# Performance work log

Hardware: AMD Instinct MI355X
Metric: run time of the kernel (lower is better)

Reference implementation:

```python
import jax, jax.numpy as jnp
import numpy as np

NEG_SLOPE = 0.2
K_L = 0.5
K_G = 0.5
TEMP_G = 1e-3


def _leaky(v):
    return jnp.where(v >= 0, v, NEG_SLOPE * v)


def _topk_row_mask(scores, keep):
    # scores: [n, n, h]; torch.topk(dim=0) -> indices [keep, n] per head,
    # then head_mask[indices, :] = 1 selects whole ROWS (any column hit).
    n = scores.shape[0]
    s = jnp.transpose(scores, (1, 2, 0))        # [n_cols, h, n_rows]
    _, idx = jax.lax.top_k(s, keep)             # [n_cols, h, keep]

    def per_head(idx_h):                        # idx_h: [n_cols, keep]
        return jnp.zeros((n,), scores.dtype).at[idx_h.reshape(-1)].set(1.0)

    rows = jax.vmap(per_head, in_axes=1, out_axes=0)(idx)  # [h, n_rows]
    return jnp.transpose(rows)[:, None, :]      # [n_rows, 1, h] broadcast over cols


def setup_inputs() -> dict:
    key = jax.random.key(0)
    ks = jax.random.split(key, 8)
    n, in_f, feat_dim = 1024, 256, 128
    H, F = 4, 64                                # n_heads, n_hidden (out_features=256)
    feats = jax.random.normal(ks[0], (n, feat_dim), dtype=jnp.float32)
    x = jax.random.normal(ks[1], (n, in_f), dtype=jnp.float32)
    adj = jax.random.randint(ks[2], (n, n, 1), 0, 2).astype(jnp.int32)
    sc = 0.05
    W_l = jax.random.normal(ks[3], (in_f, H * F), dtype=jnp.float32) * sc
    W_r = jax.random.normal(ks[4], (in_f, H * F), dtype=jnp.float32) * sc
    attn_w = jax.random.normal(ks[5], (F,), dtype=jnp.float32) * sc
    W_delta = jax.random.normal(ks[6], (2 * F, F), dtype=jnp.float32) * sc
    b_delta = jnp.zeros((F,), dtype=jnp.float32)
    return {"feats": feats, "x": x, "adj": adj, "W_l": W_l, "W_r": W_r,
            "attn_w": attn_w, "W_delta": W_delta, "b_delta": b_delta}


def reference(feats, x, adj, W_l, W_r, attn_w, W_delta, b_delta):
    n = x.shape[0]
    F = attn_w.shape[0]
    H = W_l.shape[1] // F
    g_l = (x @ W_l).reshape(n, H, F)
    g_r = (x @ W_r).reshape(n, H, F)
    # g_sum[i, j] = g_l[j] + g_r[i]  (repeat vs repeat_interleave ordering)
    g_sum = g_r[:, None, :, :] + g_l[None, :, :, :]          # [n, n, H, F]
    e = jnp.einsum('ijhf,f->ijh', _leaky(g_sum), attn_w)     # [n, n, H]

    mask_adj = adj > 0                                        # [n, n, 1]
    a_l = jax.nn.softmax(jnp.where(mask_adj, e, -jnp.inf), axis=1)
    a_1nd = a_l * mask_adj.astype(e.dtype)

    keep_l = int(n * (1.0 - K_L))
    a_filt = a_1nd * _topk_row_mask(a_1nd, keep_l)
    attn_local = jnp.einsum('ijh,jhf->ihf', a_filt, g_r)     # [n, H, F]

    omega = jax.nn.softmax(e, axis=1)
    fn = (feats - feats.min(axis=0)) / (feats.max(axis=0) - feats.min(axis=0))
    fn = jnp.where(jnp.isnan(fn), 0.0, fn)
    g_rn = (g_r - g_r.min(axis=0)) / (g_r.max(axis=0) - g_r.min(axis=0))
    nf = jnp.linalg.norm(fn, axis=1)                          # [n] (index j)
    ng = jnp.linalg.norm(g_rn, axis=2)                        # [n, H] (index i)
    alpha = jax.nn.softmax(jnp.abs(nf[None, :, None] - ng[:, None, :]), axis=1)
    gamma = 0.5 * (omega + (1.0 - alpha))

    keep_g = int(n * (1.0 - K_G))
    gf = gamma * _topk_row_mask(gamma, keep_g)
    gf = jax.nn.softmax(jnp.where(gf == 0, 1e-10, gf) / TEMP_G, axis=1)
    attn_global = jnp.einsum('ijh,jhf->ihf', gf, g_r)         # [n, H, F]

    inter = _leaky(jnp.concatenate([attn_local, attn_global], axis=2) @ W_delta + b_delta)
    delta = jax.nn.softmax(inter, axis=1)                     # softmax over heads (torch dim=1)
    attn_res = delta * attn_local + (1.0 - delta) * attn_global
    return attn_res.reshape(n, H * F)
```

## Files before the change

### kernel.cpp

```cpp
#include <hip/hip_runtime.h>
#include <cstdint>
#include <cstddef>

#define N 1024
#define HN 4
#define FDIM 64
#define KSEL 512
#define FLT_MAX_ 3.402823466e+38f

__device__ __forceinline__ float wred_sum(float v){
#pragma unroll
  for(int o=32;o>0;o>>=1) v += __shfl_down(v,o,64);
  return v;
}
__device__ __forceinline__ float bfly_sum(float v){
#pragma unroll
  for(int o=1;o<64;o<<=1) v += __shfl_xor(v,o,64);
  return v;
}
__device__ __forceinline__ float bfly_max(float v){
#pragma unroll
  for(int o=1;o<64;o<<=1) v = fmaxf(v,__shfl_xor(v,o,64));
  return v;
}
__device__ __forceinline__ float bred_sum(float v, float* scr){
  int t=threadIdx.x;
  v = wred_sum(v);
  __syncthreads();
  if((t&63)==0) scr[t>>6]=v;
  __syncthreads();
  return (scr[0]+scr[1])+(scr[2]+scr[3]);
}

__global__ __launch_bounds__(256) void stage1(const float* __restrict__ x,
                                              const float* __restrict__ W_l,
                                              const float* __restrict__ W_r,
                                              const int* __restrict__ adj,
                                              const float* __restrict__ feats,
                                              float* __restrict__ g_l,
                                              float* __restrict__ g_r,
                                              unsigned* __restrict__ adjbit,
                                              int* __restrict__ masks,
                                              float* __restrict__ pmin_f,
                                              float* __restrict__ pmax_f){
  int bx = blockIdx.x, t = threadIdx.x;
  if(bx < 512){
    const float* __restrict__ W = (bx >= 256) ? W_r : W_l;
    float* __restrict__ g = (bx >= 256) ? g_r : g_l;
    int i0 = (bx & 255)*4;
    float acc[4] = {0.f,0.f,0.f,0.f};
#pragma unroll 8
    for(int k=0;k<256;k++){
      float w = W[(size_t)k*256 + t];
#pragma unroll
      for(int r=0;r<4;r++) acc[r] = fmaf(x[(size_t)(i0+r)*256 + k], w, acc[r]);
    }
#pragma unroll
    for(int r=0;r<4;r++) g[(size_t)(i0+r)*256 + t] = acc[r];
  } else if(bx < 1536){
    int i = bx - 512, w = t>>6, lane = t&63;
    if(i < 32) masks[i*256 + t] = 0;
#pragma unroll
    for(int it=0; it<4; it++){
      int j = w*256 + it*64 + lane;
      int v = adj[(size_t)i*N + j];
      unsigned long long mb = __ballot(v > 0);
      if(lane == 0){
        adjbit[i*32 + w*8 + it*2]     = (unsigned)mb;
        adjbit[i*32 + w*8 + it*2 + 1] = (unsigned)(mb >> 32);
      }
    }
  } else {
    int chunk = bx - 1536;
    if(t < 128){
      float lo = FLT_MAX_, hi = -FLT_MAX_;
      int r0 = chunk*64;
      for(int r=0;r<64;r++){
        float v = feats[(size_t)(r0+r)*128 + t];
        lo = fminf(lo,v); hi = fmaxf(hi,v);
      }
      pmin_f[chunk*128+t]=lo; pmax_f[chunk*128+t]=hi;
    }
  }
}

__global__ __launch_bounds__(256) void stage2(const float* __restrict__ g_l,
                                              const float* __restrict__ g_r,
                                              const float* __restrict__ attn_w,
                                              const float* __restrict__ feats,
                                              const float* __restrict__ pmin_f, const float* __restrict__ pmax_f,
                                              float* __restrict__ pmin_g, float* __restrict__ pmax_g,
                                              float* __restrict__ psum_g,
                                              float* __restrict__ nf,
                                              float* __restrict__ e,
                                              float* __restrict__ eT){
  __shared__ __align__(16) float smem[2*64*68 + 128];
  int bx = blockIdx.x, t = threadIdx.x;
  if(bx < 1024){
    float* grs = smem;
    float* gls = smem + 64*68;
    float* aw  = smem + 2*64*68;
    float* aw2 = aw + 64;
    int h = bx >> 8, i0 = ((bx>>4)&15)*64, j0 = (bx&15)*64;
    if(t < 64){ float w = attn_w[t]; aw[t]=w; aw2[t]=0.2f*w; }
#pragma unroll
    for(int k=0;k<4;k++){
      int v = t + k*256;
      int r = v >> 4, f4 = (v & 15)*4;
      *(float4*)&grs[r*68 + f4] = *(const float4*)&g_r[(size_t)(i0+r)*256 + h*64 + f4];
      *(float4*)&gls[r*68 + f4] = *(const float4*)&g_l[(size_t)(j0+r)*256 + h*64 + f4];
    }
    __syncthreads();
    int tj = t&15, ti = t>>4;
    float acc[4][4];
#pragma unroll
    for(int a=0;a<4;a++)
#pragma unroll
      for(int b=0;b<4;b++) acc[a][b]=0.f;
    for(int fc=0; fc<64; fc+=4){
      float4 wv  = *(float4*)&aw[fc];
      float4 wv2 = *(float4*)&aw2[fc];
      float4 ga4[4], gb4[4];
#pragma unroll
      for(int a=0;a<4;a++) ga4[a] = *(float4*)&grs[(ti*4+a)*68+fc];
#pragma unroll
      for(int b=0;b<4;b++) gb4[b] = *(float4*)&gls[(tj+16*b)*68+fc];
#pragma unroll
      for(int a=0;a<4;a++)
#pragma unroll
        for(int b=0;b<4;b++){
          float s0 = ga4[a].x + gb4[b].x;
          float s1 = ga4[a].y + gb4[b].y;
          float s2 = ga4[a].z + gb4[b].z;
          float s3 = ga4[a].w + gb4[b].w;
          acc[a][b] = fmaf(s0, (s0>=0.f)?wv.x:wv2.x, acc[a][b]);
          acc[a][b] = fmaf(s1, (s1>=0.f)?wv.y:wv2.y, acc[a][b]);
          acc[a][b] = fmaf(s2, (s2>=0.f)?wv.z:wv2.z, acc[a][b]);
          acc[a][b] = fmaf(s3, (s3>=0.f)?wv.w:wv2.w, acc[a][b]);
        }
    }
#pragma unroll
    for(int a=0;a<4;a++)
#pragma unroll
      for(int b=0;b<4;b++){
        int i = i0 + ti*4 + a, j = j0 + tj + 16*b;
        e[((size_t)h*N + i)*N + j] = acc[a][b];
      }
    __syncthreads();
    float* esT = smem;
#pragma unroll
    for(int a=0;a<4;a++)
#pragma unroll
      for(int b=0;b<4;b++)
        esT[(tj + 16*b)*68 + ti*4 + a] = acc[a][b];
    __syncthreads();
#pragma unroll
    for(int k=0;k<4;k++){
      int jl = (t>>4) + 16*k, ilx = (t&15)*4;
      *(float4*)(eT + ((size_t)h*N + j0 + jl)*N + i0 + ilx) = *(float4*)&esT[jl*68 + ilx];
    }
  } else if(bx < 1040){
    int chunk = bx - 1024;
    float lo = FLT_MAX_, hi = -FLT_MAX_, sm = 0.f;
    int r0 = chunk*64;
    for(int r=0;r<64;r++){
      float v = g_r[(size_t)(r0+r)*256 + t];
      lo = fminf(lo,v); hi = fmaxf(hi,v); sm += v;
    }
    pmin_g[chunk*256+t]=lo; pmax_g[chunk*256+t]=hi; psum_g[chunk*256+t]=sm;
  } else {
    int i = bx - 1040;
    float* scr = smem;
    float u = 0.f;
    if(t < 128){
      float lo = FLT_MAX_, hi = -FLT_MAX_;
#pragma unroll
      for(int k=0;k<16;k++){
        lo = fminf(lo, pmin_f[k*128+t]);
        hi = fmaxf(hi, pmax_f[k*128+t]);
      }
      float d = hi - lo;
      float v = feats[(size_t)i*128 + t];
      u = (d==0.f) ? 0.f : (v - lo)/d;
    }
    float tot = bred_sum(u*u, scr);
    if(t==0) nf[i] = sqrtf(tot);
  }
}

__global__ __launch_bounds__(256) void row_stats(const float* __restrict__ e,
                                                 const unsigned* __restrict__ adjbit,
                                                 const float* __restrict__ nf,
                                                 const float* __restrict__ g_r,
                                                 const float* __restrict__ pmin_g, const float* __restrict__ pmax_g,
                                                 float* __restrict__ ng,
                                                 float* __restrict__ mlA, float* __restrict__ islA,
                                                 float* __restrict__ moA, float* __restrict__ isoA,
                                                 float* __restrict__ maA, float* __restrict__ isaA,
                                                 float* __restrict__ mgA, float* __restrict__ sgA){
  int i = blockIdx.x, t = threadIdx.x, h = t>>6, lane = t&63;
  float glo = FLT_MAX_, ghi = -FLT_MAX_;
#pragma unroll
  for(int k=0;k<16;k++){
    glo = fminf(glo, pmin_g[k*256 + h*64 + lane]);
    ghi = fmaxf(ghi, pmax_g[k*256 + h*64 + lane]);
  }
  float dg = ghi - glo;
  float ug = (g_r[(size_t)i*256 + h*64 + lane] - glo)/dg;
  float ngv = sqrtf(bfly_sum(ug*ug));
  if(lane==0) ng[h*N + i] = ngv;

  size_t base = ((size_t)h*N + i)*N;
  float er[16], nfr[16];
  unsigned nib[4];
#pragma unroll
  for(int c=0;c<4;c++){
    float4 e4 = *(const float4*)(e  + base + c*256 + lane*4);
    float4 n4 = *(const float4*)(nf + c*256 + lane*4);
    er[c*4+0]=e4.x; er[c*4+1]=e4.y; er[c*4+2]=e4.z; er[c*4+3]=e4.w;
    nfr[c*4+0]=n4.x; nfr[c*4+1]=n4.y; nfr[c*4+2]=n4.z; nfr[c*4+3]=n4.w;
    nib[c] = (adjbit[i*32 + c*8 + (lane>>3)] >> ((lane&7)*4)) & 0xFu;
  }
  float ml=-FLT_MAX_, mo=-FLT_MAX_, ma=-FLT_MAX_;
#pragma unroll
  for(int c=0;c<4;c++)
#pragma unroll
    for(int k=0;k<4;k++){
      int q = c*4+k;
      float ev = er[q];
      mo = fmaxf(mo, ev);
      if((nib[c]>>k)&1) ml = fmaxf(ml, ev);
      ma = fmaxf(ma, fabsf(nfr[q]-ngv));
    }
#pragma unroll
  for(int o=1;o<64;o<<=1){
    ml = fmaxf(ml, __shfl_xor(ml,o,64));
    mo = fmaxf(mo, __shfl_xor(mo,o,64));
    ma = fmaxf(ma, __shfl_xor(ma,o,64));
  }
  float sl=0.f, so=0.f, sa=0.f;
#pragma unroll
  for(int c=0;c<4;c++)
#pragma unroll
    for(int k=0;k<4;k++){
      int q = c*4+k;
      float ev = er[q];
      so += __expf(ev-mo);
      if((nib[c]>>k)&1) sl += __expf(ev-ml);
      sa += __expf(fabsf(nfr[q]-ngv)-ma);
    }
#pragma unroll
  for(int o=1;o<64;o<<=1){
    sl += __shfl_xor(sl,o,64);
    so += __shfl_xor(so,o,64);
    sa += __shfl_xor(sa,o,64);
  }
  float isl = 1.f/sl, iso = 1.f/so, isa = 1.f/sa;
  float gg[16];
  float mg = -FLT_MAX_;
#pragma unroll
  for(int q=0;q<16;q++){
    float ev = er[q];
    float omega = __expf(ev-mo)*iso;
    float alpha = __expf(fabsf(nfr[q]-ngv)-ma)*isa;
    float g = 0.5f*(omega + 1.f - alpha);
    gg[q] = g;
    mg = fmaxf(mg, g);
  }
  mg = bfly_max(mg);
  float sg = 0.f;
#pragma unroll
  for(int q=0;q<16;q++) sg += __expf((gg[q]-mg)/1e-3f);
  sg = bfly_sum(sg);
  if(lane==0){
    mlA[h*N+i]=ml; islA[h*N+i]=isl;
    moA[h*N+i]=mo; isoA[h*N+i]=iso;
    maA[h*N+i]=ma; isaA[h*N+i]=isa;
    mgA[h*N+i]=mg; sgA[h*N+i]=sg;
  }
}

__device__ __forceinline__ void apply_mask(const unsigned* ur, unsigned T, int tneed, int EQ,
                                           int* __restrict__ mask, int base, int lane){
  if(EQ == tneed){
#pragma unroll
    for(int c=0;c<4;c++)
#pragma unroll
      for(int k2=0;k2<4;k2++){
        int i = c*256 + lane*4 + k2;
        if(ur[c*4+k2] >= T) mask[base + i] = 1;
      }
  } else {
    int run_base = 0;
#pragma unroll
    for(int c=0;c<4;c++){
      unsigned long long bm[4];
#pragma unroll
      for(int k2=0;k2<4;k2++) bm[k2] = __ballot(ur[c*4+k2]==T);
      unsigned long long lower = (lane==0) ? 0ull : (~0ull >> (64-lane));
      int run = run_base;
#pragma unroll
      for(int k2=0;k2<4;k2++) run += (int)__popcll(bm[k2] & lower);
#pragma unroll
      for(int k2=0;k2<4;k2++){
        int i = c*256 + lane*4 + k2;
        unsigned u = ur[c*4+k2];
        bool sel = (u > T) || (u == T && run < tneed);
        run += (u==T)?1:0;
        if(sel) mask[base + i] = 1;
      }
      int ctot = 0;
#pragma unroll
      for(int k2=0;k2<4;k2++) ctot += (int)__popcll(bm[k2]);
      run_base += ctot;
    }
  }
}

__device__ __forceinline__ void run_select(const unsigned* ur, int* __restrict__ mask,
                                           int base, int lane){
  unsigned prefix = 0u;
  for(int b=30; b>=0; b--){
    unsigned cand = prefix | (1u<<b);
    int c = 0;
#pragma unroll
    for(int q=0;q<16;q++) c += (int)__popcll(__ballot(ur[q] >= cand));
    prefix = (c >= KSEL) ? cand : prefix;
  }
  unsigned T = prefix;
  int GT = 0, EQ = 0;
#pragma unroll
  for(int q=0;q<16;q++){
    GT += (int)__popcll(__ballot(ur[q] > T));
    EQ += (int)__popcll(__ballot(ur[q] == T));
  }
  int tneed = KSEL - GT;
  apply_mask(ur, T, tneed, EQ, mask, base, lane);
}

__global__ __launch_bounds__(256) void mm_sel(const float* __restrict__ eT,
                                              const float* __restrict__ g_r,
                                              const unsigned* __restrict__ adjbit,
                                              const float* __restrict__ nf,
                                              const float* __restrict__ mlA, const float* __restrict__ islA,
                                              const float* __restrict__ moA, const float* __restrict__ isoA,
                                              const float* __restrict__ maA, const float* __restrict__ isaA,
                                              const float* __restrict__ ngA,
                                              const float* __restrict__ mgA, const float* __restrict__ sgA,
                                              float* __restrict__ partL,
                                              float* __restrict__ partG,
                                              int* __restrict__ mask_l,
                                              int* __restrict__ mask_g){
  __shared__ __align__(16) float a_t[32][36];
  __shared__ __align__(16) float p_t[32][36];
  __shared__ __align__(16) float b_s[32][68];
  int bx = blockIdx.x, h = blockIdx.y, s = blockIdx.z;
  int t = threadIdx.x;

  if(bx < 64){
    int w = t>>6, lane = t&63;
    int sid = bx + 64*(h + 4*s);
    int gcol = sid*4 + w;
    int z  = gcol >> 12;
    int hj = gcol & 4095;
    int hh = hj >> 10, jc = hj & 1023;
    const float* __restrict__ src = eT + (size_t)hj * (size_t)N;

    float ev[16];
#pragma unroll
    for(int c=0;c<4;c++){
      float4 e4 = ((const float4*)src)[c*64 + lane];
      ev[c*4+0]=e4.x; ev[c*4+1]=e4.y; ev[c*4+2]=e4.z; ev[c*4+3]=e4.w;
    }
    unsigned ur[16];
    if(z == 0){
      int wo = jc >> 5; unsigned bm = 1u << (jc & 31);
#pragma unroll
      for(int c=0;c<4;c++){
        int ib = (hh<<10) + c*256 + lane*4;
        float4 ml4 = *(const float4*)(mlA+ib);
        float4 il4 = *(const float4*)(islA+ib);
        float mlv[4] = {ml4.x,ml4.y,ml4.z,ml4.w};
        float ilv[4] = {il4.x,il4.y,il4.z,il4.w};
#pragma unroll
        for(int k=0;k<4;k++){
          int i = c*256 + lane*4 + k;
          float a = (adjbit[i*32 + wo] & bm) ? __expf(ev[c*4+k]-mlv[k])*ilv[k] : 0.f;
          ur[c*4+k] = __float_as_uint(a);
        }
      }
      run_select(ur, mask_l, hh<<10, lane);
    } else {
      float nfv = nf[jc];
#pragma unroll
      for(int c=0;c<4;c++){
        int ib = (hh<<10) + c*256 + lane*4;
        float4 mo4 = *(const float4*)(moA+ib);
        float4 io4 = *(const float4*)(isoA+ib);
        float4 ma4 = *(const float4*)(maA+ib);
        float4 ia4 = *(const float4*)(isaA+ib);
        float4 ng4 = *(const float4*)(ngA+ib);
        float mov[4]={mo4.x,mo4.y,mo4.z,mo4.w}, iov[4]={io4.x,io4.y,io4.z,io4.w};
        float mav[4]={ma4.x,ma4.y,ma4.z,ma4.w}, iav[4]={ia4.x,ia4.y,ia4.z,ia4.w};
        float ngv[4]={ng4.x,ng4.y,ng4.z,ng4.w};
#pragma unroll
        for(int k=0;k<4;k++){
          float omega = __expf(ev[c*4+k]-mov[k])*iov[k];
          float alpha = __expf(fabsf(nfv-ngv[k])-mav[k])*iav[k];
          float g = 0.5f*(omega + 1.f - alpha);
          ur[c*4+k] = __float_as_uint(g);
        }
      }
      run_select(ur, mask_g, hh<<10, lane);
    }
    return;
  }

  int i0 = (bx-64)*32, j0 = s*128;
  int il = t & 31, jq = t >> 5;
  int gi = h*N + i0 + il;
  float ml_r = mlA[gi], il_r = islA[gi];
  float mo_r = moA[gi], io_r = isoA[gi];
  float ma_r = maA[gi], ia_r = isaA[gi];
  float ng_r = ngA[gi];
  float mg_r = mgA[gi], isg_r = 1.f/sgA[gi];
  int fq = t & 15, iq = t >> 4;
  int jb2a = t>>4, d4a = t&15;
  int idxb = t + 256, jb2b = idxb>>4, d4b = idxb&15;

  float e0,e1,e2,e3; unsigned aw; float4 nf4, vb0, vb1;
  {
    int jb = j0;
    size_t ebase = ((size_t)h*N + jb + jq*4)*(size_t)N + i0 + il;
    e0 = eT[ebase]; e1 = eT[ebase+N]; e2 = eT[ebase+2*N]; e3 = eT[ebase+3*N];
    aw = adjbit[(size_t)(i0+il)*32 + s*4 + 0];
    nf4 = *(const float4*)(nf + jb + jq*4);
    vb0 = *(const float4*)(g_r + (size_t)(jb+jb2a)*256 + h*64 + d4a*4);
    vb1 = *(const float4*)(g_r + (size_t)(jb+jb2b)*256 + h*64 + d4b*4);
  }
  float4 accL[2], accG[2];
#pragma unroll
  for(int r=0;r<2;r++){ accL[r]=make_float4(0,0,0,0); accG[r]=make_float4(0,0,0,0); }

  for(int sub=0; sub<4; sub++){
    __syncthreads();
    {
      float evs[4] = {e0,e1,e2,e3};
      float nfsv[4] = {nf4.x,nf4.y,nf4.z,nf4.w};
#pragma unroll
      for(int c=0;c<4;c++){
        int jl = jq*4 + c;
        float a = ((aw >> jl) & 1u) ? __expf(evs[c]-ml_r)*il_r : 0.f;
        float omega = __expf(evs[c]-mo_r)*io_r;
        float alpha = __expf(fabsf(nfsv[c]-ng_r)-ma_r)*ia_r;
        float g = 0.5f*(omega + 1.f - alpha);
        float p = __expf((g-mg_r)/1e-3f)*isg_r;
        a_t[jl][il] = a;
        p_t[jl][il] = p;
      }
      *(float4*)&b_s[jb2a][d4a*4] = vb0;
      *(float4*)&b_s[jb2b][d4b*4] = vb1;
    }
    if(sub < 3){
      int jb = j0 + (sub+1)*32;
      size_t ebase = ((size_t)h*N + jb + jq*4)*(size_t)N + i0 + il;
      e0 = eT[ebase]; e1 = eT[ebase+N]; e2 = eT[ebase+2*N]; e3 = eT[ebase+3*N];
      aw = adjbit[(size_t)(i0+il)*32 + s*4 + sub + 1];
      nf4 = *(const float4*)(nf + jb + jq*4);
      vb0 = *(const float4*)(g_r + (size_t)(jb+jb2a)*256 + h*64 + d4a*4);
      vb1 = *(const float4*)(g_r + (size_t)(jb+jb2b)*256 + h*64 + d4b*4);
    }
    __syncthreads();
#pragma unroll 8
    for(int j=0;j<32;j++){
      float4 bv = *(float4*)&b_s[j][fq*4];
      float2 av = *(float2*)&a_t[j][iq*2];
      float2 pv = *(float2*)&p_t[j][iq*2];
      accL[0].x = fmaf(av.x, bv.x, accL[0].x); accL[0].y = fmaf(av.x, bv.y, accL[0].y);
      accL[0].z = fmaf(av.x, bv.z, accL[0].z); accL[0].w = fmaf(av.x, bv.w, accL[0].w);
      accL[1].x = fmaf(av.y, bv.x, accL[1].x); accL[1].y = fmaf(av.y, bv.y, accL[1].y);
      accL[1].z = fmaf(av.y, bv.z, accL[1].z); accL[1].w = fmaf(av.y, bv.w, accL[1].w);
      accG[0].x = fmaf(pv.x, bv.x, accG[0].x); accG[0].y = fmaf(pv.x, bv.y, accG[0].y);
      accG[0].z = fmaf(pv.x, bv.z, accG[0].z); accG[0].w = fmaf(pv.x, bv.w, accG[0].w);
      accG[1].x = fmaf(pv.y, bv.x, accG[1].x); accG[1].y = fmaf(pv.y, bv.y, accG[1].y);
      accG[1].z = fmaf(pv.y, bv.z, accG[1].z); accG[1].w = fmaf(pv.y, bv.w, accG[1].w);
    }
  }
#pragma unroll
  for(int r=0;r<2;r++){
    int i = i0 + iq*2 + r;
    size_t o = ((size_t)s*N + i)*256 + h*64 + fq*4;
    *(float4*)&partL[o] = accL[r];
    *(float4*)&partG[o] = accG[r];
  }
}

__global__ __launch_bounds__(256) void epilogue(const float* __restrict__ partL,
                                                const float* __restrict__ partG,
                                                const int* __restrict__ mask_l,
                                                const int* __restrict__ mask_g,
                                                const float* __restrict__ psum_g,
                                                const float* __restrict__ W_delta,
                                                const float* __restrict__ b_delta,
                                                float* __restrict__ out){
  __shared__ float cat[4][128];
  __shared__ float inter_s[4][64];
  int i = blockIdx.x, t = threadIdx.x;
  int h = t>>6, f = t&63;
  float sl = 0.f, sg = 0.f;
#pragma unroll
  for(int s2=0;s2<8;s2++){
    size_t o = ((size_t)s2*N + i)*256 + h*64 + f;
    sl += partL[o];
    sg += partG[o];
  }
  if(!mask_l[h*N + i]) sl = 0.f;
  if(!mask_g[h*N + i]){
    float gs = 0.f;
#pragma unroll
    for(int k=0;k<16;k++) gs += psum_g[k*256 + t];
    sg = gs * (1.f/1024.f);
  }
  cat[h][f]      = sl;
  cat[h][64 + f] = sg;
  __syncthreads();
  float d = b_delta[f];
#pragma unroll 8
  for(int c=0;c<128;c++) d = fmaf(cat[h][c], W_delta[(size_t)c*64 + f], d);
  d = (d >= 0.f) ? d : 0.2f*d;
  inter_s[h][f] = d;
  __syncthreads();
  float m = inter_s[0][f];
#pragma unroll
  for(int hh=1;hh<4;hh++) m = fmaxf(m, inter_s[hh][f]);
  float ssum = 0.f;
#pragma unroll
  for(int hh=0;hh<4;hh++) ssum += __expf(inter_s[hh][f]-m);
  float delta = __expf(d - m)/ssum;
  out[(size_t)i*256 + h*64 + f] = delta*sl + (1.f - delta)*sg;
}

extern "C" void kernel_launch(void* const* d_in, const int* in_sizes, int n_in,
                              void* d_out, int out_size, void* d_ws, size_t ws_size,
                              hipStream_t stream) {
  const float* feats  = (const float*)d_in[0];
  const float* x      = (const float*)d_in[1];
  const int*   adj    = (const int*)  d_in[2];
  const float* W_l    = (const float*)d_in[3];
  const float* W_r    = (const float*)d_in[4];
  const float* attn_w = (const float*)d_in[5];
  const float* W_delta= (const float*)d_in[6];
  const float* b_delta= (const float*)d_in[7];
  float* out = (float*)d_out;

  float* ws = (float*)d_ws;
  size_t off = 0;
  float* g_l   = ws+off; off += (size_t)N*256;
  float* g_r   = ws+off; off += (size_t)N*256;
  float* e     = ws+off; off += (size_t)HN*N*N;
  float* eT    = ws+off; off += (size_t)HN*N*N;
  float* partL = ws+off; off += (size_t)8*N*256;
  float* partG = ws+off; off += (size_t)8*N*256;
  float* pmin_f= ws+off; off += 16*128;
  float* pmax_f= ws+off; off += 16*128;
  float* pmin_g= ws+off; off += 16*256;
  float* pmax_g= ws+off; off += 16*256;
  float* psum_g= ws+off; off += 16*256;
  float* nf    = ws+off; off += N;
  float* ng    = ws+off; off += (size_t)HN*N;
  float* mlA   = ws+off; off += (size_t)HN*N;
  float* islA  = ws+off; off += (size_t)HN*N;
  float* moA   = ws+off; off += (size_t)HN*N;
  float* isoA  = ws+off; off += (size_t)HN*N;
  float* maA   = ws+off; off += (size_t)HN*N;
  float* isaA  = ws+off; off += (size_t)HN*N;
  float* mgA   = ws+off; off += (size_t)HN*N;
  float* sgA   = ws+off; off += (size_t)HN*N;
  int* mask_l  = (int*)(ws+off); off += (size_t)HN*N;
  int* mask_g  = (int*)(ws+off); off += (size_t)HN*N;
  unsigned* adjbit = (unsigned*)(ws+off); off += (size_t)N*32;

  stage1<<<1552, 256, 0, stream>>>(x, W_l, W_r, adj, feats, g_l, g_r, adjbit, mask_l, pmin_f, pmax_f);

  stage2<<<2064, 256, 0, stream>>>(g_l, g_r, attn_w, feats, pmin_f, pmax_f,
                                   pmin_g, pmax_g, psum_g, nf, e, eT);

  row_stats<<<N, 256, 0, stream>>>(e, adjbit, nf, g_r, pmin_g, pmax_g, ng,
                                   mlA, islA, moA, isoA, maA, isaA, mgA, sgA);

  mm_sel<<<dim3(96,HN,8), 256, 0, stream>>>(eT, g_r, adjbit, nf,
                                            mlA, islA, moA, isoA, maA, isaA, ng,
                                            mgA, sgA, partL, partG, mask_l, mask_g);

  epilogue<<<N, 256, 0, stream>>>(partL, partG, mask_l, mask_g, psum_g, W_delta, b_delta, out);
}
```

Before: 184.6 us.

## Add transposed adjacency bitmask, stage e stores through LDS, reorder mm_sel blocks

Builds a column-major adjacency bitmask in extra stage2 blocks so the selection path in mm_sel reads one coalesced word per 32 rows instead of a strided bit per row. The row-major e tile is now staged in shared memory and written as float4 alongside eT, replacing scattered scalar stores. mm_sel's block ordering is flipped so matmul blocks get the low indices and selection blocks the high ones. This adds 16 blocks that reread the full int adjacency matrix and a second bitmask buffer.

```diff
diff --git a/kernel.cpp b/kernel.cpp
--- a/kernel.cpp
+++ b/kernel.cpp
@@ -88,10 +88,12 @@
                                               const float* __restrict__ g_r,
                                               const float* __restrict__ attn_w,
                                               const float* __restrict__ feats,
+                                              const int* __restrict__ adj,
                                               const float* __restrict__ pmin_f, const float* __restrict__ pmax_f,
                                               float* __restrict__ pmin_g, float* __restrict__ pmax_g,
                                               float* __restrict__ psum_g,
                                               float* __restrict__ nf,
+                                              unsigned* __restrict__ adjbitT,
                                               float* __restrict__ e,
                                               float* __restrict__ eT){
   __shared__ __align__(16) float smem[2*64*68 + 128];
@@ -139,25 +141,22 @@
           acc[a][b] = fmaf(s3, (s3>=0.f)?wv.w:wv2.w, acc[a][b]);
         }
     }
+    __syncthreads();
+    float* es  = smem;
+    float* esT = smem + 64*68;
 #pragma unroll
     for(int a=0;a<4;a++)
 #pragma unroll
       for(int b=0;b<4;b++){
-        int i = i0 + ti*4 + a, j = j0 + tj + 16*b;
-        e[((size_t)h*N + i)*N + j] = acc[a][b];
+        es [(ti*4+a)*68 + (tj+16*b)] = acc[a][b];
+        esT[(tj+16*b)*68 + (ti*4+a)] = acc[a][b];
       }
     __syncthreads();
-    float* esT = smem;
-#pragma unroll
-    for(int a=0;a<4;a++)
-#pragma unroll
-      for(int b=0;b<4;b++)
-        esT[(tj + 16*b)*68 + ti*4 + a] = acc[a][b];
-    __syncthreads();
 #pragma unroll
     for(int k=0;k<4;k++){
-      int jl = (t>>4) + 16*k, ilx = (t&15)*4;
-      *(float4*)(eT + ((size_t)h*N + j0 + jl)*N + i0 + ilx) = *(float4*)&esT[jl*68 + ilx];
+      int rl = (t>>4) + 16*k, cl4 = (t&15)*4;
+      *(float4*)(e  + ((size_t)h*N + i0 + rl)*N + j0 + cl4) = *(float4*)&es [rl*68 + cl4];
+      *(float4*)(eT + ((size_t)h*N + j0 + rl)*N + i0 + cl4) = *(float4*)&esT[rl*68 + cl4];
     }
   } else if(bx < 1040){
     int chunk = bx - 1024;
@@ -168,7 +167,7 @@
       lo = fminf(lo,v); hi = fmaxf(hi,v); sm += v;
     }
     pmin_g[chunk*256+t]=lo; pmax_g[chunk*256+t]=hi; psum_g[chunk*256+t]=sm;
-  } else {
+  } else if(bx < 2064){
     int i = bx - 1040;
     float* scr = smem;
     float u = 0.f;
@@ -185,6 +184,19 @@
     }
     float tot = bred_sum(u*u, scr);
     if(t==0) nf[i] = sqrtf(tot);
+  } else {
+    int B = bx - 2064, j0 = B*64;
+    int w = t>>6, lane = t&63;
+    unsigned word = 0u;
+    for(int ii=0; ii<256; ii++){
+      int i = w*256 + ii;
+      int v = adj[(size_t)i*N + j0 + lane];
+      word |= (v > 0 ? 1u : 0u) << (ii & 31);
+      if((ii & 31) == 31){
+        adjbitT[(size_t)(j0+lane)*32 + (i>>5)] = word;
+        word = 0u;
+      }
+    }
   }
 }
 
@@ -341,6 +353,7 @@
 __global__ __launch_bounds__(256) void mm_sel(const float* __restrict__ eT,
                                               const float* __restrict__ g_r,
                                               const unsigned* __restrict__ adjbit,
+                                              const unsigned* __restrict__ adjbitT,
                                               const float* __restrict__ nf,
                                               const float* __restrict__ mlA, const float* __restrict__ islA,
                                               const float* __restrict__ moA, const float* __restrict__ isoA,
@@ -357,9 +370,9 @@
   int bx = blockIdx.x, h = blockIdx.y, s = blockIdx.z;
   int t = threadIdx.x;
 
-  if(bx < 64){
+  if(bx >= 32){
     int w = t>>6, lane = t&63;
-    int sid = bx + 64*(h + 4*s);
+    int sid = (bx - 32) + 64*(h + 4*s);
     int gcol = sid*4 + w;
     int z  = gcol >> 12;
     int hj = gcol & 4095;
@@ -374,9 +387,10 @@
     }
     unsigned ur[16];
     if(z == 0){
-      int wo = jc >> 5; unsigned bm = 1u << (jc & 31);
+      size_t tbase = (size_t)jc*32;
 #pragma unroll
       for(int c=0;c<4;c++){
+        unsigned awT = adjbitT[tbase + c*8 + (lane>>3)];
         int ib = (hh<<10) + c*256 + lane*4;
         float4 ml4 = *(const float4*)(mlA+ib);
         float4 il4 = *(const float4*)(islA+ib);
@@ -384,8 +398,7 @@
         float ilv[4] = {il4.x,il4.y,il4.z,il4.w};
 #pragma unroll
         for(int k=0;k<4;k++){
-          int i = c*256 + lane*4 + k;
-          float a = (adjbit[i*32 + wo] & bm) ? __expf(ev[c*4+k]-mlv[k])*ilv[k] : 0.f;
+          float a = ((awT >> ((lane&7)*4 + k)) & 1u) ? __expf(ev[c*4+k]-mlv[k])*ilv[k] : 0.f;
           ur[c*4+k] = __float_as_uint(a);
         }
       }
@@ -416,7 +429,7 @@
     return;
   }
 
-  int i0 = (bx-64)*32, j0 = s*128;
+  int i0 = bx*32, j0 = s*128;
   int il = t & 31, jq = t >> 5;
   int gi = h*N + i0 + il;
   float ml_r = mlA[gi], il_r = islA[gi];
@@ -578,17 +591,18 @@
   float* sgA   = ws+off; off += (size_t)HN*N;
   int* mask_l  = (int*)(ws+off); off += (size_t)HN*N;
   int* mask_g  = (int*)(ws+off); off += (size_t)HN*N;
-  unsigned* adjbit = (unsigned*)(ws+off); off += (size_t)N*32;
+  unsigned* adjbit  = (unsigned*)(ws+off); off += (size_t)N*32;
+  unsigned* adjbitT = (unsigned*)(ws+off); off += (size_t)N*32;
 
   stage1<<<1552, 256, 0, stream>>>(x, W_l, W_r, adj, feats, g_l, g_r, adjbit, mask_l, pmin_f, pmax_f);
 
-  stage2<<<2064, 256, 0, stream>>>(g_l, g_r, attn_w, feats, pmin_f, pmax_f,
-                                   pmin_g, pmax_g, psum_g, nf, e, eT);
+  stage2<<<2080, 256, 0, stream>>>(g_l, g_r, attn_w, feats, adj, pmin_f, pmax_f,
+                                   pmin_g, pmax_g, psum_g, nf, adjbitT, e, eT);
 
   row_stats<<<N, 256, 0, stream>>>(e, adjbit, nf, g_r, pmin_g, pmax_g, ng,
                                    mlA, islA, moA, isoA, maA, isaA, mgA, sgA);
 
-  mm_sel<<<dim3(96,HN,8), 256, 0, stream>>>(eT, g_r, adjbit, nf,
+  mm_sel<<<dim3(96,HN,8), 256, 0, stream>>>(eT, g_r, adjbit, adjbitT, nf,
                                             mlA, islA, moA, isoA, maA, isaA, ng,
                                             mgA, sgA, partL, partG, mask_l, mask_g);
 
```

After: 196.6 us. 6.5% more time.
